# Performance work log

Hardware: AMD Instinct MI355X
Metric: run time of the kernel (lower is better)

Reference implementation:

```python
import jax, jax.numpy as jnp
import numpy as np
from jax import lax

INPUT_DIM = 16
H1 = 5
H2 = 50
NUM_CLASSES = 20
B = 4096
T = 512


def _lstm(x, w_ih, w_hh, b_ih, b_hh, hidden):
    # x: [B, T, D]; PyTorch LSTM gate order i, f, g, o; returns all hidden states [B, T, H]
    xg = jnp.einsum('btd,gd->btg', x, w_ih) + (b_ih + b_hh)  # [B, T, 4H]
    xg_t = jnp.swapaxes(xg, 0, 1)  # [T, B, 4H]
    h0 = jnp.zeros((x.shape[0], hidden), x.dtype)
    c0 = jnp.zeros((x.shape[0], hidden), x.dtype)

    def step(carry, xt):
        h, c = carry
        g = xt + h @ w_hh.T  # [B, 4H]
        i, f, gg, o = jnp.split(g, 4, axis=-1)
        i = jax.nn.sigmoid(i)
        f = jax.nn.sigmoid(f)
        gg = jnp.tanh(gg)
        o = jax.nn.sigmoid(o)
        c = f * c + i * gg
        h = o * jnp.tanh(c)
        return (h, c), h

    _, hs = lax.scan(step, (h0, c0), xg_t)
    return jnp.swapaxes(hs, 0, 1)  # [B, T, H]


def setup_inputs() -> dict:
    key = jax.random.key(0)
    ks = jax.random.split(key, 12)
    s1 = 1.0 / np.sqrt(H1)
    s2 = 1.0 / np.sqrt(H2)
    u = lambda k, shape, s: jax.random.uniform(k, shape, jnp.float32, -s, s)
    return {
        'x': jax.random.normal(ks[0], (B, T, INPUT_DIM), jnp.float32),
        'w_ih1': u(ks[1], (4 * H1, INPUT_DIM), s1),
        'w_hh1': u(ks[2], (4 * H1, H1), s1),
        'b_ih1': u(ks[3], (4 * H1,), s1),
        'b_hh1': u(ks[4], (4 * H1,), s1),
        'w_ih2': u(ks[5], (4 * H2, H1), s2),
        'w_hh2': u(ks[6], (4 * H2, H2), s2),
        'b_ih2': u(ks[7], (4 * H2,), s2),
        'b_hh2': u(ks[8], (4 * H2,), s2),
        'fc_w': u(ks[9], (NUM_CLASSES, H2), s2),
        'fc_b': u(ks[10], (NUM_CLASSES,), s2),
    }


def reference(x, w_ih1, w_hh1, b_ih1, b_hh1, w_ih2, w_hh2, b_ih2, b_hh2, fc_w, fc_b):
    h1 = _lstm(x, w_ih1, w_hh1, b_ih1, b_hh1, H1)   # [B, T, 5]
    h2 = _lstm(h1, w_ih2, w_hh2, b_ih2, b_hh2, H2)  # [B, T, 50]
    feat = h2[:, -1, :]  # last timestep; dropout is identity in eval mode
    out = feat @ fc_w.T + fc_b  # [B, num_classes]
    return (out, feat)
```

## Files before the change

kernel.cpp:

```cpp
#include <hip/hip_runtime.h>
#include <stdint.h>

#define B_TOTAL 4096
#define T_STEPS 512
#define IN_DIM 16
#define H1 5
#define H2 50
#define NCLS 20

typedef __attribute__((ext_vector_type(8))) short bf16x8;
typedef __attribute__((ext_vector_type(4))) float f32x4;

#define LOG2E 1.44269504f
#define C2L   2.88539008f
#define C2L2  5.77078016f

__device__ inline float rcp1pexp2(float y){
  return __builtin_amdgcn_rcpf(1.0f + __builtin_amdgcn_exp2f(y));
}

__device__ inline void split1(float h, unsigned short& hi, unsigned short& lo){
  unsigned u = __float_as_uint(h);
  hi = (unsigned short)(u >> 16);
  float r = h - __uint_as_float(u & 0xFFFF0000u);
  lo = (unsigned short)(__float_as_uint(r) >> 16);
}
__device__ inline void wsplit(float w, short& hi, short& lo){
  unsigned u = __float_as_uint(w);
  hi = (short)(u >> 16);
  float r = w - __uint_as_float(u & 0xFFFF0000u);
  lo = (short)(__float_as_uint(r) >> 16);
}
__device__ inline void xsplit(float4 a, float4 b, bf16x8& H, bf16x8& L){
  short h,l;
  wsplit(a.x,h,l); H[0]=h; L[0]=l;
  wsplit(a.y,h,l); H[1]=h; L[1]=l;
  wsplit(a.z,h,l); H[2]=h; L[2]=l;
  wsplit(a.w,h,l); H[3]=h; L[3]=l;
  wsplit(b.x,h,l); H[4]=h; L[4]=l;
  wsplit(b.y,h,l); H[5]=h; L[5]=l;
  wsplit(b.z,h,l); H[6]=h; L[6]=l;
  wsplit(b.w,h,l); H[7]=h; L[7]=l;
}

#define LDS_FENCE() __asm__ volatile("s_waitcnt lgkmcnt(0)" ::: "memory")
#define BARRIER()   __asm__ volatile("s_barrier" ::: "memory")

__global__ __launch_bounds__(256, 1) void lstm_fused_kernel(
    const float* __restrict__ x,
    const float* __restrict__ w_ih1, const float* __restrict__ w_hh1,
    const float* __restrict__ b_ih1, const float* __restrict__ b_hh1,
    const float* __restrict__ w_ih2, const float* __restrict__ w_hh2,
    const float* __restrict__ b_ih2, const float* __restrict__ b_hh2,
    const float* __restrict__ fc_w, const float* __restrict__ fc_b,
    float* __restrict__ out)
{
  const int tid  = threadIdx.x;
  const int lane = tid & 63;
  const int wave = tid >> 6;
  const int l15  = lane & 15;
  const int quad = lane >> 4;
  const int b0   = blockIdx.x * 16;

  __shared__ __align__(16) unsigned short a2h[2][16*72], a2l[2][16*72];
  __shared__ float h2f[16*52];

  const bf16x8 zero8 = {0,0,0,0,0,0,0,0};
  const f32x4  zero4 = {0.f,0.f,0.f,0.f};

  bf16x8 Bh[4][3], Bl[4][3];
  f32x4 biasv[4];
  float cst[4] = {0.f,0.f,0.f,0.f};

#pragma unroll
  for (int tt=0; tt<4; ++tt)
#pragma unroll
    for (int kt=0; kt<3; ++kt){ Bh[tt][kt]=zero8; Bl[tt][kt]=zero8; }

  if (wave < 3){
    const int c = wave*16 + l15;
#pragma unroll
    for (int tt=0; tt<4; ++tt){
      const float gsc = (tt == 2) ? C2L : LOG2E;
      const int grow = tt*H2 + c;
#pragma unroll
      for (int kt=0; kt<2; ++kt){
#pragma unroll
        for (int j=0;j<8;j++){
          const int kk = kt*32 + quad*8 + j;
          float w = 0.f;
          if (kk < H2)         w = w_hh2[grow*H2 + kk];
          else if (kk < H2+H1) w = w_ih2[grow*H1 + (kk-H2)];
          w *= gsc;
          short hi, lo; wsplit(w, hi, lo);
          Bh[tt][kt][j] = hi; Bl[tt][kt][j] = lo;
        }
      }
      const float bias = gsc * (b_ih2[grow] + b_hh2[grow]);
      biasv[tt][0]=bias; biasv[tt][1]=bias; biasv[tt][2]=bias; biasv[tt][3]=bias;
    }
  } else {
#pragma unroll
    for (int tt=0; tt<4; ++tt){
      const float gsc = (tt == 2) ? C2L : LOG2E;
      float bias = 0.f;
      if (l15 < 2){
        const int grow = tt*H2 + 48 + l15;
#pragma unroll
        for (int kt=0; kt<2; ++kt){
#pragma unroll
          for (int j=0;j<8;j++){
            const int kk = kt*32 + quad*8 + j;
            float w = 0.f;
            if (kk < H2)         w = w_hh2[grow*H2 + kk];
            else if (kk < H2+H1) w = w_ih2[grow*H1 + (kk-H2)];
            w *= gsc;
            short hi, lo; wsplit(w, hi, lo);
            Bh[tt][kt][j] = hi; Bl[tt][kt][j] = lo;
          }
        }
        bias = gsc * (b_ih2[grow] + b_hh2[grow]);
      } else if (l15 < 7){
        const int e = l15 - 2;
        const int grow = tt*H1 + e;
#pragma unroll
        for (int j=0;j<8;j++){
          const int kk = 32 + quad*8 + j;
          float w1 = (kk >= H2 && kk < H2+H1) ? gsc * w_hh1[grow*H1 + (kk-H2)] : 0.f;
          short hi, lo; wsplit(w1, hi, lo);
          Bh[tt][1][j] = hi; Bl[tt][1][j] = lo;
          const int k2 = quad*8 + j;
          float w2 = (k2 < IN_DIM) ? gsc * w_ih1[grow*IN_DIM + k2] : 0.f;
          wsplit(w2, hi, lo);
          Bh[tt][2][j] = hi; Bl[tt][2][j] = lo;
        }
        bias = gsc * (b_ih1[grow] + b_hh1[grow]);
      }
      biasv[tt][0]=bias; biasv[tt][1]=bias; biasv[tt][2]=bias; biasv[tt][3]=bias;
    }
  }

  { unsigned short* p = &a2h[0][0]; for (int i=tid;i<2*16*72;i+=256) p[i]=0; }
  { unsigned short* p = &a2l[0][0]; for (int i=tid;i<2*16*72;i+=256) p[i]=0; }

  bf16x8 XAh = zero8, XAl = zero8, XBh = zero8, XBl = zero8;
  float4 pa, pb;
  const bool xact = (wave == 3) && (quad < 2);
  const float* xbase = &x[(size_t)(b0+l15)*T_STEPS*IN_DIM + quad*8];
  if (xact){
    float4 a0 = *(const float4*)(xbase + 0);
    float4 a1 = *(const float4*)(xbase + 4);
    xsplit(a0, a1, XAh, XAl);
    pa = *(const float4*)(xbase + 1*IN_DIM);
    pb = *(const float4*)(xbase + 1*IN_DIM + 4);
  }
  __syncthreads();

#define ROTATE(XH_, XL_, SN_) do { \
    if (xact){ \
      xsplit(pa, pb, XH_, XL_); \
      const int sn_ = (SN_) < T_STEPS ? (SN_) : T_STEPS-1; \
      const float* xp_ = xbase + (size_t)sn_*IN_DIM; \
      pa = *(const float4*)xp_; \
      pb = *(const float4*)(xp_ + 4); \
    } } while(0)

#define ACT_BLOCK(ACC_, HV_) \
    _Pragma("unroll") \
    for (int r=0;r<4;r++){ \
      float gi = rcp1pexp2(-ACC_[0][r]); \
      float gf = rcp1pexp2(-ACC_[1][r]); \
      float gg = fmaf(-C2L2, rcp1pexp2(ACC_[2][r]), C2L);  \
      float go = rcp1pexp2(-ACC_[3][r]); \
      cst[r] = fmaf(gf, cst[r], gi * gg); \
      HV_[r] = go * fmaf(-2.0f, rcp1pexp2(cst[r]), 1.0f); \
    }

#define MAIN_BODY(T_, RD_, WR_, XCH_, XCL_, XNH_, XNL_) do { \
    const int rb_ = l15*72; \
    bf16x8 ah0 = *(const bf16x8*)&a2h[RD_][rb_ +      quad*8]; \
    bf16x8 al0 = *(const bf16x8*)&a2l[RD_][rb_ +      quad*8]; \
    bf16x8 ah1 = *(const bf16x8*)&a2h[RD_][rb_ + 32 + quad*8]; \
    bf16x8 al1 = *(const bf16x8*)&a2l[RD_][rb_ + 32 + quad*8]; \
    if (wave == 3) ROTATE(XNH_, XNL_, (T_)+3);   \
    f32x4 acc[4]; \
    if (wave < 3){ \
      _Pragma("unroll") \
      for (int tt=0; tt<4; ++tt){ \
        f32x4 c0 = __builtin_amdgcn_mfma_f32_16x16x32_bf16(ah0, Bh[tt][0], biasv[tt], 0,0,0); \
        c0 = __builtin_amdgcn_mfma_f32_16x16x32_bf16(al0, Bh[tt][0], c0, 0,0,0); \
        c0 = __builtin_amdgcn_mfma_f32_16x16x32_bf16(ah0, Bl[tt][0], c0, 0,0,0); \
        f32x4 c1 = __builtin_amdgcn_mfma_f32_16x16x32_bf16(ah1, Bh[tt][1], zero4, 0,0,0); \
        c1 = __builtin_amdgcn_mfma_f32_16x16x32_bf16(al1, Bh[tt][1], c1, 0,0,0); \
        c1 = __builtin_amdgcn_mfma_f32_16x16x32_bf16(ah1, Bl[tt][1], c1, 0,0,0); \
        acc[tt] = c0 + c1; \
      } \
    } else { \
      _Pragma("unroll") \
      for (int tt=0; tt<4; ++tt){ \
        f32x4 c0 = __builtin_amdgcn_mfma_f32_16x16x32_bf16(ah0, Bh[tt][0], biasv[tt], 0,0,0); \
        c0 = __builtin_amdgcn_mfma_f32_16x16x32_bf16(al0, Bh[tt][0], c0, 0,0,0); \
        c0 = __builtin_amdgcn_mfma_f32_16x16x32_bf16(ah0, Bl[tt][0], c0, 0,0,0); \
        f32x4 c1 = __builtin_amdgcn_mfma_f32_16x16x32_bf16(ah1, Bh[tt][1], zero4, 0,0,0); \
        c1 = __builtin_amdgcn_mfma_f32_16x16x32_bf16(al1, Bh[tt][1], c1, 0,0,0); \
        c1 = __builtin_amdgcn_mfma_f32_16x16x32_bf16(ah1, Bl[tt][1], c1, 0,0,0); \
        f32x4 c2 = __builtin_amdgcn_mfma_f32_16x16x32_bf16(XCH_, Bh[tt][2], zero4, 0,0,0); \
        c2 = __builtin_amdgcn_mfma_f32_16x16x32_bf16(XCL_, Bh[tt][2], c2, 0,0,0); \
        c2 = __builtin_amdgcn_mfma_f32_16x16x32_bf16(XCH_, Bl[tt][2], c2, 0,0,0); \
        acc[tt] = (c0 + c1) + c2; \
      } \
    } \
    float hv[4]; \
    ACT_BLOCK(acc, hv) \
    if (wave < 3){ \
      const int wrb = quad*4*72 + wave*16 + l15; \
      _Pragma("unroll") \
      for (int r=0;r<4;r++){ \
        unsigned short hh, hl; split1(hv[r], hh, hl); \
        a2h[WR_][wrb + r*72] = hh; \
        a2l[WR_][wrb + r*72] = hl; \
      } \
      if ((T_) == T_STEPS-1){ \
        _Pragma("unroll") \
        for (int r=0;r<4;r++){ \
          out[(size_t)B_TOTAL*NCLS + (size_t)(b0+quad*4+r)*H2 + wave*16+l15] = hv[r]; \
          h2f[(quad*4+r)*52 + wave*16+l15] = hv[r]; \
        } \
      } \
    } else if (l15 < 7){ \
      const int wrb = quad*4*72 + 48 + l15;   \
      _Pragma("unroll") \
      for (int r=0;r<4;r++){ \
        unsigned short hh, hl; split1(hv[r], hh, hl); \
        a2h[WR_][wrb + r*72] = hh; \
        a2l[WR_][wrb + r*72] = hl; \
      } \
      if ((T_) == T_STEPS-1 && l15 < 2){ \
        _Pragma("unroll") \
        for (int r=0;r<4;r++){ \
          out[(size_t)B_TOTAL*NCLS + (size_t)(b0+quad*4+r)*H2 + 48+l15] = hv[r]; \
          h2f[(quad*4+r)*52 + 48+l15] = hv[r]; \
        } \
      } \
    } \
  } while(0)

  if (wave == 3){
    f32x4 acc[4];
#pragma unroll
    for (int tt=0; tt<4; ++tt){
      f32x4 c2 = __builtin_amdgcn_mfma_f32_16x16x32_bf16(XAh, Bh[tt][2], biasv[tt], 0,0,0);
      c2 = __builtin_amdgcn_mfma_f32_16x16x32_bf16(XAl, Bh[tt][2], c2, 0,0,0);
      c2 = __builtin_amdgcn_mfma_f32_16x16x32_bf16(XAh, Bl[tt][2], c2, 0,0,0);
      acc[tt] = c2;
    }
    ROTATE(XBh, XBl, 2);
    const bool isl1 = (l15 >= 2) && (l15 < 7);
#pragma unroll
    for (int r=0;r<4;r++){
      float gi = rcp1pexp2(-acc[0][r]);
      float gf = rcp1pexp2(-acc[1][r]);
      float gg = fmaf(-C2L2, rcp1pexp2(acc[2][r]), C2L);
      float go = rcp1pexp2(-acc[3][r]);
      float cn = fmaf(gf, cst[r], gi * gg);
      if (isl1){
        cst[r] = cn;
        float h = go * fmaf(-2.0f, rcp1pexp2(cn), 1.0f);
        unsigned short hh, hl; split1(h, hh, hl);
        const int row = quad*4 + r;
        a2h[0][row*72 + 48 + l15] = hh;
        a2l[0][row*72 + 48 + l15] = hl;
      }
    }
  }
  LDS_FENCE(); BARRIER();

  for (int t2 = 0; t2 < T_STEPS; t2 += 2){
    MAIN_BODY(t2,   0, 1, XBh, XBl, XAh, XAl);
    LDS_FENCE(); BARRIER();
    MAIN_BODY(t2+1, 1, 0, XAh, XAl, XBh, XBl);
    LDS_FENCE(); BARRIER();
  }

#undef MAIN_BODY
#undef ACT_BLOCK
#undef ROTATE

  __syncthreads();
  for (int i = tid; i < 16*NCLS; i += 256){
    const int b = i / NCLS, o = i % NCLS;
    float s = fc_b[o];
#pragma unroll 10
    for (int k=0;k<H2;k++) s += fc_w[o*H2+k] * h2f[b*52+k];
    out[(size_t)(b0+b)*NCLS + o] = s;
  }
}

extern "C" void kernel_launch(void* const* d_in, const int* in_sizes, int n_in,
                              void* d_out, int out_size, void* d_ws, size_t ws_size,
                              hipStream_t stream) {
  const float* x     = (const float*)d_in[0];
  const float* w_ih1 = (const float*)d_in[1];
  const float* w_hh1 = (const float*)d_in[2];
  const float* b_ih1 = (const float*)d_in[3];
  const float* b_hh1 = (const float*)d_in[4];
  const float* w_ih2 = (const float*)d_in[5];
  const float* w_hh2 = (const float*)d_in[6];
  const float* b_ih2 = (const float*)d_in[7];
  const float* b_hh2 = (const float*)d_in[8];
  const float* fc_w  = (const float*)d_in[9];
  const float* fc_b  = (const float*)d_in[10];
  float* out = (float*)d_out;

  lstm_fused_kernel<<<dim3(B_TOTAL/16), dim3(256), 0, stream>>>(
      x, w_ih1, w_hh1, b_ih1, b_hh1, w_ih2, w_hh2, b_ih2, b_hh2, fc_w, fc_b, out);
}
```

Baseline: 605.1 us.

## Halve batch rows per block and stage x through LDS via producer lanes

Each block now handles 8 batch rows instead of 16, which doubles the grid to 512 blocks, and launch bounds allow two blocks per CU. Input x is prefetched by half of wave 0, split to bf16 hi/lo with perm packing, and staged in double-buffered LDS, replacing the wave-3 register rotation. The aim is to fill more CUs and overlap two blocks' serial recurrences. In exchange, half the MFMA rows are wasted on padding and the register budget is tighter.

```diff
diff --git a/kernel.cpp b/kernel.cpp
--- a/kernel.cpp
+++ b/kernel.cpp
@@ -7,6 +7,8 @@
 #define H1 5
 #define H2 50
 #define NCLS 20
+#define BATCH 8
+#define XFS 40
 
 typedef __attribute__((ext_vector_type(8))) short bf16x8;
 typedef __attribute__((ext_vector_type(4))) float f32x4;
@@ -19,6 +21,21 @@
   return __builtin_amdgcn_rcpf(1.0f + __builtin_amdgcn_exp2f(y));
 }
 
+__device__ inline unsigned pack_top(float a, float b){
+  return __builtin_amdgcn_perm(__float_as_uint(a), __float_as_uint(b), 0x07060302u);
+}
+__device__ inline void cvt_store(unsigned short* dh, unsigned short* dl, float4 v){
+  uint2 H, L;
+  H.x = pack_top(v.y, v.x);
+  H.y = pack_top(v.w, v.z);
+  float r0 = v.x - __uint_as_float(__float_as_uint(v.x) & 0xFFFF0000u);
+  float r1 = v.y - __uint_as_float(__float_as_uint(v.y) & 0xFFFF0000u);
+  float r2 = v.z - __uint_as_float(__float_as_uint(v.z) & 0xFFFF0000u);
+  float r3 = v.w - __uint_as_float(__float_as_uint(v.w) & 0xFFFF0000u);
+  L.x = pack_top(r1, r0);
+  L.y = pack_top(r3, r2);
+  *(uint2*)dh = H; *(uint2*)dl = L;
+}
 __device__ inline void split1(float h, unsigned short& hi, unsigned short& lo){
   unsigned u = __float_as_uint(h);
   hi = (unsigned short)(u >> 16);
@@ -46,7 +63,7 @@
 #define LDS_FENCE() __asm__ volatile("s_waitcnt lgkmcnt(0)" ::: "memory")
 #define BARRIER()   __asm__ volatile("s_barrier" ::: "memory")
 
-__global__ __launch_bounds__(256, 1) void lstm_fused_kernel(
+__global__ __launch_bounds__(256, 2) void lstm_fused_kernel(
     const float* __restrict__ x,
     const float* __restrict__ w_ih1, const float* __restrict__ w_hh1,
     const float* __restrict__ b_ih1, const float* __restrict__ b_hh1,
@@ -60,10 +77,11 @@
   const int wave = tid >> 6;
   const int l15  = lane & 15;
   const int quad = lane >> 4;
-  const int b0   = blockIdx.x * 16;
+  const int b0   = blockIdx.x * BATCH;
 
   __shared__ __align__(16) unsigned short a2h[2][16*72], a2l[2][16*72];
-  __shared__ float h2f[16*52];
+  __shared__ __align__(16) unsigned short xfh[2][16*XFS], xfl[2][16*XFS];
+  __shared__ float h2f[BATCH*52];
 
   const bf16x8 zero8 = {0,0,0,0,0,0,0,0};
   const f32x4  zero4 = {0.f,0.f,0.f,0.f};
@@ -140,112 +158,29 @@
     }
   }
 
-  { unsigned short* p = &a2h[0][0]; for (int i=tid;i<2*16*72;i+=256) p[i]=0; }
-  { unsigned short* p = &a2l[0][0]; for (int i=tid;i<2*16*72;i+=256) p[i]=0; }
-
-  bf16x8 XAh = zero8, XAl = zero8, XBh = zero8, XBl = zero8;
-  float4 pa, pb;
-  const bool xact = (wave == 3) && (quad < 2);
-  const float* xbase = &x[(size_t)(b0+l15)*T_STEPS*IN_DIM + quad*8];
-  if (xact){
-    float4 a0 = *(const float4*)(xbase + 0);
-    float4 a1 = *(const float4*)(xbase + 4);
-    xsplit(a0, a1, XAh, XAl);
-    pa = *(const float4*)(xbase + 1*IN_DIM);
-    pb = *(const float4*)(xbase + 1*IN_DIM + 4);
-  }
+  { unsigned short* p = &a2h[0][0]; for (int i=tid;i<2*16*72;i+=256)  p[i]=0; }
+  { unsigned short* p = &a2l[0][0]; for (int i=tid;i<2*16*72;i+=256)  p[i]=0; }
+  { unsigned short* p = &xfh[0][0]; for (int i=tid;i<2*16*XFS;i+=256) p[i]=0; }
+  { unsigned short* p = &xfl[0][0]; for (int i=tid;i<2*16*XFS;i+=256) p[i]=0; }
   __syncthreads();
 
-#define ROTATE(XH_, XL_, SN_) do { \
-    if (xact){ \
-      xsplit(pa, pb, XH_, XL_); \
-      const int sn_ = (SN_) < T_STEPS ? (SN_) : T_STEPS-1; \
-      const float* xp_ = xbase + (size_t)sn_*IN_DIM; \
-      pa = *(const float4*)xp_; \
-      pb = *(const float4*)(xp_ + 4); \
-    } } while(0)
-
-#define ACT_BLOCK(ACC_, HV_) \
-    _Pragma("unroll") \
-    for (int r=0;r<4;r++){ \
-      float gi = rcp1pexp2(-ACC_[0][r]); \
-      float gf = rcp1pexp2(-ACC_[1][r]); \
-      float gg = fmaf(-C2L2, rcp1pexp2(ACC_[2][r]), C2L);  \
-      float go = rcp1pexp2(-ACC_[3][r]); \
-      cst[r] = fmaf(gf, cst[r], gi * gg); \
-      HV_[r] = go * fmaf(-2.0f, rcp1pexp2(cst[r]), 1.0f); \
-    }
-
-#define MAIN_BODY(T_, RD_, WR_, XCH_, XCL_, XNH_, XNL_) do { \
-    const int rb_ = l15*72; \
-    bf16x8 ah0 = *(const bf16x8*)&a2h[RD_][rb_ +      quad*8]; \
-    bf16x8 al0 = *(const bf16x8*)&a2l[RD_][rb_ +      quad*8]; \
-    bf16x8 ah1 = *(const bf16x8*)&a2h[RD_][rb_ + 32 + quad*8]; \
-    bf16x8 al1 = *(const bf16x8*)&a2l[RD_][rb_ + 32 + quad*8]; \
-    if (wave == 3) ROTATE(XNH_, XNL_, (T_)+3);   \
-    f32x4 acc[4]; \
-    if (wave < 3){ \
-      _Pragma("unroll") \
-      for (int tt=0; tt<4; ++tt){ \
-        f32x4 c0 = __builtin_amdgcn_mfma_f32_16x16x32_bf16(ah0, Bh[tt][0], biasv[tt], 0,0,0); \
-        c0 = __builtin_amdgcn_mfma_f32_16x16x32_bf16(al0, Bh[tt][0], c0, 0,0,0); \
-        c0 = __builtin_amdgcn_mfma_f32_16x16x32_bf16(ah0, Bl[tt][0], c0, 0,0,0); \
-        f32x4 c1 = __builtin_amdgcn_mfma_f32_16x16x32_bf16(ah1, Bh[tt][1], zero4, 0,0,0); \
-        c1 = __builtin_amdgcn_mfma_f32_16x16x32_bf16(al1, Bh[tt][1], c1, 0,0,0); \
-        c1 = __builtin_amdgcn_mfma_f32_16x16x32_bf16(ah1, Bl[tt][1], c1, 0,0,0); \
-        acc[tt] = c0 + c1; \
-      } \
-    } else { \
-      _Pragma("unroll") \
-      for (int tt=0; tt<4; ++tt){ \
-        f32x4 c0 = __builtin_amdgcn_mfma_f32_16x16x32_bf16(ah0, Bh[tt][0], biasv[tt], 0,0,0); \
-        c0 = __builtin_amdgcn_mfma_f32_16x16x32_bf16(al0, Bh[tt][0], c0, 0,0,0); \
-        c0 = __builtin_amdgcn_mfma_f32_16x16x32_bf16(ah0, Bl[tt][0], c0, 0,0,0); \
-        f32x4 c1 = __builtin_amdgcn_mfma_f32_16x16x32_bf16(ah1, Bh[tt][1], zero4, 0,0,0); \
-        c1 = __builtin_amdgcn_mfma_f32_16x16x32_bf16(al1, Bh[tt][1], c1, 0,0,0); \
-        c1 = __builtin_amdgcn_mfma_f32_16x16x32_bf16(ah1, Bl[tt][1], c1, 0,0,0); \
-        f32x4 c2 = __builtin_amdgcn_mfma_f32_16x16x32_bf16(XCH_, Bh[tt][2], zero4, 0,0,0); \
-        c2 = __builtin_amdgcn_mfma_f32_16x16x32_bf16(XCL_, Bh[tt][2], c2, 0,0,0); \
-        c2 = __builtin_amdgcn_mfma_f32_16x16x32_bf16(XCH_, Bl[tt][2], c2, 0,0,0); \
-        acc[tt] = (c0 + c1) + c2; \
-      } \
-    } \
-    float hv[4]; \
-    ACT_BLOCK(acc, hv) \
-    if (wave < 3){ \
-      const int wrb = quad*4*72 + wave*16 + l15; \
-      _Pragma("unroll") \
-      for (int r=0;r<4;r++){ \
-        unsigned short hh, hl; split1(hv[r], hh, hl); \
-        a2h[WR_][wrb + r*72] = hh; \
-        a2l[WR_][wrb + r*72] = hl; \
-      } \
-      if ((T_) == T_STEPS-1){ \
-        _Pragma("unroll") \
-        for (int r=0;r<4;r++){ \
-          out[(size_t)B_TOTAL*NCLS + (size_t)(b0+quad*4+r)*H2 + wave*16+l15] = hv[r]; \
-          h2f[(quad*4+r)*52 + wave*16+l15] = hv[r]; \
-        } \
-      } \
-    } else if (l15 < 7){ \
-      const int wrb = quad*4*72 + 48 + l15;   \
-      _Pragma("unroll") \
-      for (int r=0;r<4;r++){ \
-        unsigned short hh, hl; split1(hv[r], hh, hl); \
-        a2h[WR_][wrb + r*72] = hh; \
-        a2l[WR_][wrb + r*72] = hl; \
-      } \
-      if ((T_) == T_STEPS-1 && l15 < 2){ \
-        _Pragma("unroll") \
-        for (int r=0;r<4;r++){ \
-          out[(size_t)B_TOTAL*NCLS + (size_t)(b0+quad*4+r)*H2 + 48+l15] = hv[r]; \
-          h2f[(quad*4+r)*52 + 48+l15] = hv[r]; \
-        } \
-      } \
-    } \
-  } while(0)
+  const bool xprod = (wave == 0) && (lane < 32);
+  const int pxb = lane >> 2;
+  const int pxd = (lane & 3) * 4;
+  const float* pxbase = &x[(size_t)(b0+pxb)*T_STEPS*IN_DIM + pxd];
+  float4 PA, PB;
+  if (xprod){
+    float4 v1 = *(const float4*)(pxbase + 1*IN_DIM);
+    cvt_store(&xfh[1][pxb*XFS+pxd], &xfl[1][pxb*XFS+pxd], v1);
+    PA = *(const float4*)(pxbase + 2*IN_DIM);
+  }
 
   if (wave == 3){
+    bf16x8 XAh = zero8, XAl = zero8;
+    if (quad < 2 && l15 < BATCH){
+      const float* xp = &x[(size_t)(b0+l15)*T_STEPS*IN_DIM + quad*8];
+      xsplit(*(const float4*)xp, *(const float4*)(xp+4), XAh, XAl);
+    }
     f32x4 acc[4];
 #pragma unroll
     for (int tt=0; tt<4; ++tt){
@@ -254,8 +189,7 @@
       c2 = __builtin_amdgcn_mfma_f32_16x16x32_bf16(XAh, Bl[tt][2], c2, 0,0,0);
       acc[tt] = c2;
     }
-    ROTATE(XBh, XBl, 2);
-    const bool isl1 = (l15 >= 2) && (l15 < 7);
+    const bool isl1 = (l15 >= 2) && (l15 < 7) && (quad < 2);
 #pragma unroll
     for (int r=0;r<4;r++){
       float gi = rcp1pexp2(-acc[0][r]);
@@ -275,19 +209,106 @@
   }
   LDS_FENCE(); BARRIER();
 
+#define ACT_BLOCK(ACC_, HV_) \
+    _Pragma("unroll") \
+    for (int r=0;r<4;r++){ \
+      float gi = rcp1pexp2(-ACC_[0][r]); \
+      float gf = rcp1pexp2(-ACC_[1][r]); \
+      float gg = fmaf(-C2L2, rcp1pexp2(ACC_[2][r]), C2L);  \
+      float go = rcp1pexp2(-ACC_[3][r]); \
+      cst[r] = fmaf(gf, cst[r], gi * gg); \
+      HV_[r] = go * fmaf(-2.0f, rcp1pexp2(cst[r]), 1.0f); \
+    }
+
+#define MAIN_BODY(T_, RD_, WR_, PXW_, PXL_) do { \
+    if (xprod){ \
+      cvt_store(&xfh[RD_][pxb*XFS+pxd], &xfl[RD_][pxb*XFS+pxd], PXW_);  \
+      const int nidx_ = ((T_)+3 < T_STEPS) ? (T_)+3 : T_STEPS-1; \
+      PXL_ = *(const float4*)(pxbase + (size_t)nidx_*IN_DIM);           \
+    } \
+    const int rb_ = l15*72; \
+    bf16x8 ah0 = *(const bf16x8*)&a2h[RD_][rb_ +      quad*8]; \
+    bf16x8 al0 = *(const bf16x8*)&a2l[RD_][rb_ +      quad*8]; \
+    bf16x8 ah1 = *(const bf16x8*)&a2h[RD_][rb_ + 32 + quad*8]; \
+    bf16x8 al1 = *(const bf16x8*)&a2l[RD_][rb_ + 32 + quad*8]; \
+    f32x4 acc[4]; \
+    if (wave < 3){ \
+      _Pragma("unroll") \
+      for (int tt=0; tt<4; ++tt){ \
+        f32x4 c0 = __builtin_amdgcn_mfma_f32_16x16x32_bf16(ah0, Bh[tt][0], biasv[tt], 0,0,0); \
+        c0 = __builtin_amdgcn_mfma_f32_16x16x32_bf16(al0, Bh[tt][0], c0, 0,0,0); \
+        c0 = __builtin_amdgcn_mfma_f32_16x16x32_bf16(ah0, Bl[tt][0], c0, 0,0,0); \
+        f32x4 c1 = __builtin_amdgcn_mfma_f32_16x16x32_bf16(ah1, Bh[tt][1], zero4, 0,0,0); \
+        c1 = __builtin_amdgcn_mfma_f32_16x16x32_bf16(al1, Bh[tt][1], c1, 0,0,0); \
+        c1 = __builtin_amdgcn_mfma_f32_16x16x32_bf16(ah1, Bl[tt][1], c1, 0,0,0); \
+        acc[tt] = c0 + c1; \
+      } \
+    } else { \
+      bf16x8 xfH = *(const bf16x8*)&xfh[WR_][l15*XFS + quad*8]; \
+      bf16x8 xfL = *(const bf16x8*)&xfl[WR_][l15*XFS + quad*8]; \
+      _Pragma("unroll") \
+      for (int tt=0; tt<4; ++tt){ \
+        f32x4 c0 = __builtin_amdgcn_mfma_f32_16x16x32_bf16(ah0, Bh[tt][0], biasv[tt], 0,0,0); \
+        c0 = __builtin_amdgcn_mfma_f32_16x16x32_bf16(al0, Bh[tt][0], c0, 0,0,0); \
+        c0 = __builtin_amdgcn_mfma_f32_16x16x32_bf16(ah0, Bl[tt][0], c0, 0,0,0); \
+        f32x4 c1 = __builtin_amdgcn_mfma_f32_16x16x32_bf16(ah1, Bh[tt][1], zero4, 0,0,0); \
+        c1 = __builtin_amdgcn_mfma_f32_16x16x32_bf16(al1, Bh[tt][1], c1, 0,0,0); \
+        c1 = __builtin_amdgcn_mfma_f32_16x16x32_bf16(ah1, Bl[tt][1], c1, 0,0,0); \
+        f32x4 c2 = __builtin_amdgcn_mfma_f32_16x16x32_bf16(xfH, Bh[tt][2], zero4, 0,0,0); \
+        c2 = __builtin_amdgcn_mfma_f32_16x16x32_bf16(xfL, Bh[tt][2], c2, 0,0,0); \
+        c2 = __builtin_amdgcn_mfma_f32_16x16x32_bf16(xfH, Bl[tt][2], c2, 0,0,0); \
+        acc[tt] = (c0 + c1) + c2; \
+      } \
+    } \
+    float hv[4]; \
+    ACT_BLOCK(acc, hv) \
+    if (wave < 3){ \
+      if (quad < 2){ \
+        const int wrb = quad*4*72 + wave*16 + l15; \
+        _Pragma("unroll") \
+        for (int r=0;r<4;r++){ \
+          unsigned short hh, hl; split1(hv[r], hh, hl); \
+          a2h[WR_][wrb + r*72] = hh; \
+          a2l[WR_][wrb + r*72] = hl; \
+        } \
+        if ((T_) == T_STEPS-1){ \
+          _Pragma("unroll") \
+          for (int r=0;r<4;r++){ \
+            out[(size_t)B_TOTAL*NCLS + (size_t)(b0+quad*4+r)*H2 + wave*16+l15] = hv[r]; \
+            h2f[(quad*4+r)*52 + wave*16+l15] = hv[r]; \
+          } \
+        } \
+      } \
+    } else if (l15 < 7 && quad < 2){ \
+      const int wrb = quad*4*72 + 48 + l15;   \
+      _Pragma("unroll") \
+      for (int r=0;r<4;r++){ \
+        unsigned short hh, hl; split1(hv[r], hh, hl); \
+        a2h[WR_][wrb + r*72] = hh; \
+        a2l[WR_][wrb + r*72] = hl; \
+      } \
+      if ((T_) == T_STEPS-1 && l15 < 2){ \
+        _Pragma("unroll") \
+        for (int r=0;r<4;r++){ \
+          out[(size_t)B_TOTAL*NCLS + (size_t)(b0+quad*4+r)*H2 + 48+l15] = hv[r]; \
+          h2f[(quad*4+r)*52 + 48+l15] = hv[r]; \
+        } \
+      } \
+    } \
+  } while(0)
+
   for (int t2 = 0; t2 < T_STEPS; t2 += 2){
-    MAIN_BODY(t2,   0, 1, XBh, XBl, XAh, XAl);
+    MAIN_BODY(t2,   0, 1, PA, PB);
     LDS_FENCE(); BARRIER();
-    MAIN_BODY(t2+1, 1, 0, XAh, XAl, XBh, XBl);
+    MAIN_BODY(t2+1, 1, 0, PB, PA);
     LDS_FENCE(); BARRIER();
   }
 
 #undef MAIN_BODY
 #undef ACT_BLOCK
-#undef ROTATE
 
   __syncthreads();
-  for (int i = tid; i < 16*NCLS; i += 256){
+  for (int i = tid; i < BATCH*NCLS; i += 256){
     const int b = i / NCLS, o = i % NCLS;
     float s = fc_b[o];
 #pragma unroll 10
@@ -312,6 +333,6 @@
   const float* fc_b  = (const float*)d_in[10];
   float* out = (float*)d_out;
 
-  lstm_fused_kernel<<<dim3(B_TOTAL/16), dim3(256), 0, stream>>>(
+  lstm_fused_kernel<<<dim3(B_TOTAL/BATCH), dim3(256), 0, stream>>>(
       x, w_ih1, w_hh1, b_ih1, b_hh1, w_ih2, w_hh2, b_ih2, b_hh2, fc_w, fc_b, out);
 }
```

Result: slower. 727.4 us (+20.2%).
